# Kernel tuning notes

Measured on AMD Instinct MI355X. Metric: run time of the kernel, lower is better.

## Reference

```python
import jax, jax.numpy as jnp
import numpy as np

OUT_FEATURES = 4096
IN_FEATURES = 4096
GROUP_SIZE = 256
NUM_GROUPS = OUT_FEATURES * IN_FEATURES // GROUP_SIZE  # 65536


def setup_inputs() -> dict:
    key = jax.random.key(0)
    k1, k2, k3 = jax.random.split(key, 3)
    x = jax.random.normal(k1, (4, 2048, IN_FEATURES), dtype=jnp.float32)
    weight_packed = jax.random.randint(k2, (NUM_GROUPS, GROUP_SIZE // 2), 0, 256, dtype=jnp.int32)
    # params[..., 0] = scale, params[..., 1] = zero_point; keep scales small like real quant params
    weight_params = jax.random.uniform(k3, (NUM_GROUPS, 2), dtype=jnp.float32) * jnp.array([0.01, 0.1], dtype=jnp.float32)
    return {"x": x, "weight_packed": weight_packed, "weight_params": weight_params}


def _dequantize_4bit(weight_packed, weight_params):
    # weight_packed: [G, gs/2] bytes, two 4-bit values per byte (low nibble = even index)
    scales = weight_params[:, 0:1]  # [G, 1]
    zeros = weight_params[:, 1:2]   # [G, 1]
    low = (weight_packed & 15).astype(jnp.float32)          # even positions
    high = ((weight_packed >> 4) & 15).astype(jnp.float32)  # odd positions
    q = jnp.stack([low, high], axis=-1).reshape(weight_packed.shape[0], -1)  # [G, gs]
    return q * scales + zeros


def reference(x, weight_packed, weight_params):
    w = _dequantize_4bit(weight_packed, weight_params)  # [G, gs]
    w = w.reshape(-1)[: OUT_FEATURES * IN_FEATURES].reshape(OUT_FEATURES, IN_FEATURES)
    # F.linear(x, W) = x @ W.T
    return jnp.einsum("bsi,oi->bso", x, w)
```

## Files before the change

kernel.cpp:

```cpp
#include <hip/hip_runtime.h>
#include <hip/hip_bf16.h>


#define M_DIM 8192
#define N_DIM 4096
#define K_DIM 4096

typedef __bf16 bf16x8 __attribute__((ext_vector_type(8)));
typedef float f32x4 __attribute__((ext_vector_type(4)));
typedef unsigned short us8 __attribute__((ext_vector_type(8)));

__device__ __forceinline__ unsigned short f2bf_rne(float f) {
    unsigned int u = __builtin_bit_cast(unsigned int, f);
    u += 0x7FFFu + ((u >> 16) & 1u);
    return (unsigned short)(u >> 16);
}

__global__ void prep_kernel(const float* __restrict__ x,
                            const int* __restrict__ packed,
                            const float* __restrict__ params,
                            ushort* __restrict__ a,
                            ushort* __restrict__ w) {
    int b = blockIdx.x;
    if (b < 16384) {
        int j = b * 256 + threadIdx.x;
        float4 v0 = ((const float4*)x)[2 * j];
        float4 v1 = ((const float4*)x)[2 * j + 1];
        us8 o;
        o[0] = f2bf_rne(v0.x); o[1] = f2bf_rne(v0.y);
        o[2] = f2bf_rne(v0.z); o[3] = f2bf_rne(v0.w);
        o[4] = f2bf_rne(v1.x); o[5] = f2bf_rne(v1.y);
        o[6] = f2bf_rne(v1.z); o[7] = f2bf_rne(v1.w);
        ((us8*)a)[j] = o;
    } else {
        int j = (b - 16384) * 256 + threadIdx.x;
        int4 v = ((const int4*)packed)[j];
        int g = j >> 5;
        float s = params[2 * g], z = params[2 * g + 1];
        unsigned int o0, o1, o2, o3;
        o0 = (unsigned int)f2bf_rne((float)(v.x & 15) * s + z)
           | ((unsigned int)f2bf_rne((float)((v.x >> 4) & 15) * s + z) << 16);
        o1 = (unsigned int)f2bf_rne((float)(v.y & 15) * s + z)
           | ((unsigned int)f2bf_rne((float)((v.y >> 4) & 15) * s + z) << 16);
        o2 = (unsigned int)f2bf_rne((float)(v.z & 15) * s + z)
           | ((unsigned int)f2bf_rne((float)((v.z >> 4) & 15) * s + z) << 16);
        o3 = (unsigned int)f2bf_rne((float)(v.w & 15) * s + z)
           | ((unsigned int)f2bf_rne((float)((v.w >> 4) & 15) * s + z) << 16);
        ((uint4*)w)[j] = make_uint4(o0, o1, o2, o3);
    }
}

__global__ __launch_bounds__(512, 2) void gemm_bt(const ushort* __restrict__ A,
                                                  const ushort* __restrict__ B,
                                                  float* __restrict__ C) {
    __shared__ ushort lds[65536];

    const int tid  = threadIdx.x;
    const int w    = tid >> 6;
    const int lane = tid & 63;
    const int quad = lane >> 4;
    const int l16  = lane & 15;
    const int wm   = w >> 2;
    const int wn   = w & 3;

    const int bid = blockIdx.x;
    const int sid = (bid & 7) * 64 + (bid >> 3);
    const int by  = sid & 31;
    const int bx  = sid >> 5;
    const int m0  = by * 256;
    const int n0  = bx * 256;

    const int srow = tid >> 3;
    const int scol = ((tid & 7) ^ (srow & 7)) * 8;
    const ushort* aS = A + (size_t)(m0 + srow) * K_DIM + scol;
    const ushort* bS = B + (size_t)(n0 + srow) * K_DIM + scol;

    f32x4 acc[8][4] = {};
    bf16x8 afA[2][2], afB[2][2];
    bf16x8 bf0a[4], bf0b[4];
    bf16x8 bf1[4];

    auto stageA = [&](int t, int h) {
        const int kc   = (t < 64 ? t : 63) * 64;
        const int slot = ((t & 1) * 2 + h) * 8192;
#pragma unroll
        for (int l = 0; l < 2; ++l)
            __builtin_amdgcn_global_load_lds(
                (const __attribute__((address_space(1))) void*)(aS + (size_t)(h * 128 + l * 64) * K_DIM + kc),
                (__attribute__((address_space(3))) void*)(lds + slot + (l * 512 + w * 64) * 8),
                16, 0, 0);
    };
    auto stageB = [&](int t, int h) {
        const int kc   = (t < 64 ? t : 63) * 64;
        const int slot = 32768 + ((t & 1) * 2 + h) * 8192;
#pragma unroll
        for (int l = 0; l < 2; ++l)
            __builtin_amdgcn_global_load_lds(
                (const __attribute__((address_space(1))) void*)(bS + (size_t)(h * 128 + l * 64) * K_DIM + kc),
                (__attribute__((address_space(3))) void*)(lds + slot + (l * 512 + w * 64) * 8),
                16, 0, 0);
    };

    const int aBase = wm * 8192;
    const int bBase = 32768 + (wn >> 1) * 8192;
    const int bR0   = (wn & 1) * 64;
    const int swz8  = l16 & 7;
    const int c0    = (quad ^ swz8) * 8;
    const int c1    = ((4 + quad) ^ swz8) * 8;
    const ushort* pA0 = lds + aBase + l16 * 64 + c0;
    const ushort* pA1 = lds + aBase + l16 * 64 + c1;
    const ushort* pB0 = lds + bBase + (bR0 + l16) * 64 + c0;
    const ushort* pB1 = lds + bBase + (bR0 + l16) * 64 + c1;

#define MFMA_PH(PH, AF, BF0)                                                   \
    do {                                                                       \
        __builtin_amdgcn_s_setprio(1);                                         \
        _Pragma("unroll")                                                      \
        for (int ii = 0; ii < 2; ++ii)                                         \
            _Pragma("unroll")                                                  \
            for (int j = 0; j < 4; ++j)                                        \
                acc[(PH) * 2 + ii][j] = __builtin_amdgcn_mfma_f32_16x16x32_bf16( \
                    AF[ii][0], BF0[j], acc[(PH) * 2 + ii][j], 0, 0, 0);        \
        _Pragma("unroll")                                                      \
        for (int ii = 0; ii < 2; ++ii)                                         \
            _Pragma("unroll")                                                  \
            for (int j = 0; j < 4; ++j)                                        \
                acc[(PH) * 2 + ii][j] = __builtin_amdgcn_mfma_f32_16x16x32_bf16( \
                    AF[ii][1], bf1[j], acc[(PH) * 2 + ii][j], 0, 0, 0);        \
        __builtin_amdgcn_s_setprio(0);                                         \
    } while (0)

#define READ_A(DST, BUF, PH)                                                   \
    do {                                                                       \
        _Pragma("unroll")                                                      \
        for (int ii = 0; ii < 2; ++ii) {                                       \
            DST[ii][0] = *(const bf16x8*)(pA0 + (BUF) + ((PH) * 32 + ii * 16) * 64); \
            DST[ii][1] = *(const bf16x8*)(pA1 + (BUF) + ((PH) * 32 + ii * 16) * 64); \
        }                                                                      \
    } while (0)
#define READ_B0(DST, BUF)                                                      \
    do {                                                                       \
        _Pragma("unroll")                                                      \
        for (int j = 0; j < 4; ++j)                                            \
            DST[j] = *(const bf16x8*)(pB0 + (BUF) + j * 1024);                 \
    } while (0)
#define READ_B1(BUF)                                                           \
    do {                                                                       \
        _Pragma("unroll")                                                      \
        for (int j = 0; j < 4; ++j)                                            \
            bf1[j] = *(const bf16x8*)(pB1 + (BUF) + j * 1024);                 \
    } while (0)

    stageB(0, 0); stageB(0, 1); stageA(0, 0); stageA(0, 1); stageB(1, 0); stageB(1, 1);
    asm volatile("s_waitcnt vmcnt(4)" ::: "memory");
    __builtin_amdgcn_s_barrier();
    asm volatile("" ::: "memory");
    READ_B0(bf0a, 0);
    READ_A(afA, 0, 0);

#define TILE(T, BUF, NBUF, BF0C, BF0N)                                         \
    do {                                                                       \
        const int t = (T);                                                     \
                                                                      \
        READ_B1(BUF);                                                          \
        READ_A(afB, BUF, 1);                                                   \
        stageA(t + 1, 0);                                                      \
        MFMA_PH(0, afA, BF0C);                                                 \
                                                                      \
        READ_A(afA, BUF, 2);                                                   \
        stageA(t + 1, 1);                                                      \
        MFMA_PH(1, afB, BF0C);                                                 \
        asm volatile("s_waitcnt lgkmcnt(8)" ::: "memory");  \
        __builtin_amdgcn_sched_barrier(0);                  \
        __builtin_amdgcn_s_barrier();                 \
        asm volatile("" ::: "memory");                                         \
                                                                      \
        READ_A(afB, BUF, 3);                                                   \
        stageB(t + 2, 0);                                                      \
        MFMA_PH(2, afA, BF0C);                                                 \
                                                                      \
        stageB(t + 2, 1);                                                      \
        asm volatile("s_waitcnt vmcnt(4) lgkmcnt(0)" ::: "memory");            \
        __builtin_amdgcn_s_barrier();                \
        asm volatile("" ::: "memory");                                         \
        if (t < 63) { READ_B0(BF0N, NBUF); READ_A(afA, NBUF, 0); }             \
        __builtin_amdgcn_sched_barrier(0);                                     \
        MFMA_PH(3, afB, BF0C);                                                 \
    } while (0)

#pragma unroll 1
    for (int tt = 0; tt < 64; tt += 2) {
        TILE(tt,     0,     16384, bf0a, bf0b);
        TILE(tt + 1, 16384, 0,     bf0b, bf0a);
    }
#undef TILE
#undef MFMA_PH
#undef READ_A
#undef READ_B0
#undef READ_B1

    const int crow = m0 + wm * 128 + quad * 4;
    const int ccol = n0 + wn * 64 + l16;
#pragma unroll
    for (int rf = 0; rf < 8; ++rf)
#pragma unroll
        for (int j = 0; j < 4; ++j)
#pragma unroll
            for (int r = 0; r < 4; ++r)
                C[(size_t)(crow + rf * 16 + r) * N_DIM + ccol + j * 16] = acc[rf][j][r];
}

__global__ void naive_kernel(const float* __restrict__ x, const int* __restrict__ packed,
                             const float* __restrict__ params, float* __restrict__ out) {
    int idx = blockIdx.x * blockDim.x + threadIdx.x;
    if (idx >= M_DIM * N_DIM) return;
    int m = idx / N_DIM, o = idx % N_DIM;
    const float* xr = x + (size_t)m * K_DIM;
    float sum = 0.f;
    for (int gi = 0; gi < K_DIM / 256; ++gi) {
        int g = o * (K_DIM / 256) + gi;
        float s = params[2 * g], z = params[2 * g + 1];
        const int* p = packed + (size_t)g * 128;
        const float* xx = xr + gi * 256;
        for (int j = 0; j < 128; ++j) {
            int v = p[j];
            sum += xx[2 * j]     * ((float)(v & 15) * s + z);
            sum += xx[2 * j + 1] * ((float)((v >> 4) & 15) * s + z);
        }
    }
    out[idx] = sum;
}

extern "C" void kernel_launch(void* const* d_in, const int* in_sizes, int n_in,
                              void* d_out, int out_size, void* d_ws, size_t ws_size,
                              hipStream_t stream) {
    const float* x      = (const float*)d_in[0];
    const int*   packed = (const int*)d_in[1];
    const float* params = (const float*)d_in[2];
    float* out = (float*)d_out;

    const size_t a_bytes = (size_t)M_DIM * K_DIM * 2;
    const size_t w_bytes = (size_t)N_DIM * K_DIM * 2;

    if (ws_size >= a_bytes + w_bytes) {
        ushort* Abf = (ushort*)d_ws;
        ushort* Wbf = (ushort*)((char*)d_ws + a_bytes);

        prep_kernel<<<24576, 256, 0, stream>>>(x, packed, params, Abf, Wbf);

        gemm_bt<<<512, 512, 0, stream>>>(Abf, Wbf, out);
    } else {
        int n = M_DIM * N_DIM;
        naive_kernel<<<(n + 255) / 256, 256, 0, stream>>>(x, packed, params, out);
    }
}
```

Before: 455.9 us.

## Switch GEMM inner loop from 16x16x32 to 32x32x16 bf16 MFMA tiles

Replaces the 16x16x32 MFMA fragments with 32x32x16 bf16 MFMA, restructuring per-wave fragments into 4x2 accumulators of 16 floats and reorganizing LDS reads per K-substep. The larger MFMA shape reduces the number of LDS fragment loads and MFMA issues per unit of work, giving each fragment more reuse. It changes register usage and the waitcnt counts. The epilogue store layout also changes to match the 32x32 output layout.

```diff
diff --git a/kernel.cpp b/kernel.cpp
--- a/kernel.cpp
+++ b/kernel.cpp
@@ -7,7 +7,7 @@
 #define K_DIM 4096
 
 typedef __bf16 bf16x8 __attribute__((ext_vector_type(8)));
-typedef float f32x4 __attribute__((ext_vector_type(4)));
+typedef float f32x16 __attribute__((ext_vector_type(16)));
 typedef unsigned short us8 __attribute__((ext_vector_type(8)));
 
 __device__ __forceinline__ unsigned short f2bf_rne(float f) {
@@ -58,8 +58,8 @@
     const int tid  = threadIdx.x;
     const int w    = tid >> 6;
     const int lane = tid & 63;
-    const int quad = lane >> 4;
-    const int l16  = lane & 15;
+    const int r32  = lane & 31;
+    const int hi   = lane >> 5;
     const int wm   = w >> 2;
     const int wn   = w & 3;
 
@@ -75,10 +75,10 @@
     const ushort* aS = A + (size_t)(m0 + srow) * K_DIM + scol;
     const ushort* bS = B + (size_t)(n0 + srow) * K_DIM + scol;
 
-    f32x4 acc[8][4] = {};
-    bf16x8 afA[2][2], afB[2][2];
-    bf16x8 bf0a[4], bf0b[4];
-    bf16x8 bf1[4];
+    f32x16 acc[4][2] = {};
+    bf16x8 afA[4], afB[4];
+    bf16x8 bf0a[2], bf0b[2];
+    bf16x8 bfk[3][2];
 
     auto stageA = [&](int t, int h) {
         const int kc   = (t < 64 ? t : 63) * 64;
@@ -104,51 +104,48 @@
     const int aBase = wm * 8192;
     const int bBase = 32768 + (wn >> 1) * 8192;
     const int bR0   = (wn & 1) * 64;
-    const int swz8  = l16 & 7;
-    const int c0    = (quad ^ swz8) * 8;
-    const int c1    = ((4 + quad) ^ swz8) * 8;
-    const ushort* pA0 = lds + aBase + l16 * 64 + c0;
-    const ushort* pA1 = lds + aBase + l16 * 64 + c1;
-    const ushort* pB0 = lds + bBase + (bR0 + l16) * 64 + c0;
-    const ushort* pB1 = lds + bBase + (bR0 + l16) * 64 + c1;
-
-#define MFMA_PH(PH, AF, BF0)                                                   \
+    const int swz   = lane & 7;
+    const ushort* pA[4];
+    const ushort* pB[4];
+#pragma unroll
+    for (int ks = 0; ks < 4; ++ks) {
+        const int c = ((ks * 2 + hi) ^ swz) * 8;
+        pA[ks] = lds + aBase + r32 * 64 + c;
+        pB[ks] = lds + bBase + (bR0 + r32) * 64 + c;
+    }
+
+#define MFMA_KS(AF, B0, B1)                                                    \
     do {                                                                       \
         __builtin_amdgcn_s_setprio(1);                                         \
         _Pragma("unroll")                                                      \
-        for (int ii = 0; ii < 2; ++ii)                                         \
-            _Pragma("unroll")                                                  \
-            for (int j = 0; j < 4; ++j)                                        \
-                acc[(PH) * 2 + ii][j] = __builtin_amdgcn_mfma_f32_16x16x32_bf16( \
-                    AF[ii][0], BF0[j], acc[(PH) * 2 + ii][j], 0, 0, 0);        \
+        for (int mi = 0; mi < 4; ++mi) {                                       \
+            acc[mi][0] = __builtin_amdgcn_mfma_f32_32x32x16_bf16(              \
+                AF[mi], B0, acc[mi][0], 0, 0, 0);                              \
+            acc[mi][1] = __builtin_amdgcn_mfma_f32_32x32x16_bf16(              \
+                AF[mi], B1, acc[mi][1], 0, 0, 0);                              \
+        }                                                                      \
+        __builtin_amdgcn_s_setprio(0);                                         \
+    } while (0)
+
+#define READ_A(DST, BUF, KS)                                                   \
+    do {                                                                       \
         _Pragma("unroll")                                                      \
-        for (int ii = 0; ii < 2; ++ii)                                         \
-            _Pragma("unroll")                                                  \
-            for (int j = 0; j < 4; ++j)                                        \
-                acc[(PH) * 2 + ii][j] = __builtin_amdgcn_mfma_f32_16x16x32_bf16( \
-                    AF[ii][1], bf1[j], acc[(PH) * 2 + ii][j], 0, 0, 0);        \
-        __builtin_amdgcn_s_setprio(0);                                         \
-    } while (0)
-
-#define READ_A(DST, BUF, PH)                                                   \
-    do {                                                                       \
-        _Pragma("unroll")                                                      \
-        for (int ii = 0; ii < 2; ++ii) {                                       \
-            DST[ii][0] = *(const bf16x8*)(pA0 + (BUF) + ((PH) * 32 + ii * 16) * 64); \
-            DST[ii][1] = *(const bf16x8*)(pA1 + (BUF) + ((PH) * 32 + ii * 16) * 64); \
-        }                                                                      \
+        for (int mi = 0; mi < 4; ++mi)                                         \
+            DST[mi] = *(const bf16x8*)(pA[KS] + (BUF) + mi * 2048);            \
     } while (0)
 #define READ_B0(DST, BUF)                                                      \
     do {                                                                       \
-        _Pragma("unroll")                                                      \
-        for (int j = 0; j < 4; ++j)                                            \
-            DST[j] = *(const bf16x8*)(pB0 + (BUF) + j * 1024);                 \
-    } while (0)
-#define READ_B1(BUF)                                                           \
-    do {                                                                       \
-        _Pragma("unroll")                                                      \
-        for (int j = 0; j < 4; ++j)                                            \
-            bf1[j] = *(const bf16x8*)(pB1 + (BUF) + j * 1024);                 \
+        DST[0] = *(const bf16x8*)(pB[0] + (BUF));                              \
+        DST[1] = *(const bf16x8*)(pB[0] + (BUF) + 2048);                       \
+    } while (0)
+#define READ_B123(BUF)                                                         \
+    do {                                                                       \
+        bfk[0][0] = *(const bf16x8*)(pB[1] + (BUF));                           \
+        bfk[0][1] = *(const bf16x8*)(pB[1] + (BUF) + 2048);                    \
+        bfk[1][0] = *(const bf16x8*)(pB[2] + (BUF));                           \
+        bfk[1][1] = *(const bf16x8*)(pB[2] + (BUF) + 2048);                    \
+        bfk[2][0] = *(const bf16x8*)(pB[3] + (BUF));                           \
+        bfk[2][1] = *(const bf16x8*)(pB[3] + (BUF) + 2048);                    \
     } while (0)
 
     stageB(0, 0); stageB(0, 1); stageA(0, 0); stageA(0, 1); stageB(1, 0); stageB(1, 1);
@@ -162,22 +159,22 @@
     do {                                                                       \
         const int t = (T);                                                     \
                                                                       \
-        READ_B1(BUF);                                                          \
+        READ_B123(BUF);                                                        \
         READ_A(afB, BUF, 1);                                                   \
         stageA(t + 1, 0);                                                      \
-        MFMA_PH(0, afA, BF0C);                                                 \
+        MFMA_KS(afA, BF0C[0], BF0C[1]);                                        \
                                                                       \
         READ_A(afA, BUF, 2);                                                   \
         stageA(t + 1, 1);                                                      \
-        MFMA_PH(1, afB, BF0C);                                                 \
-        asm volatile("s_waitcnt lgkmcnt(8)" ::: "memory");  \
+        MFMA_KS(afB, bfk[0][0], bfk[0][1]);                                    \
+        asm volatile("s_waitcnt lgkmcnt(4)" ::: "memory");  \
         __builtin_amdgcn_sched_barrier(0);                  \
         __builtin_amdgcn_s_barrier();                 \
         asm volatile("" ::: "memory");                                         \
                                                                       \
         READ_A(afB, BUF, 3);                                                   \
         stageB(t + 2, 0);                                                      \
-        MFMA_PH(2, afA, BF0C);                                                 \
+        MFMA_KS(afA, bfk[1][0], bfk[1][1]);                                    \
                                                                       \
         stageB(t + 2, 1);                                                      \
         asm volatile("s_waitcnt vmcnt(4) lgkmcnt(0)" ::: "memory");            \
@@ -185,7 +182,7 @@
         asm volatile("" ::: "memory");                                         \
         if (t < 63) { READ_B0(BF0N, NBUF); READ_A(afA, NBUF, 0); }             \
         __builtin_amdgcn_sched_barrier(0);                                     \
-        MFMA_PH(3, afB, BF0C);                                                 \
+        MFMA_KS(afB, bfk[2][0], bfk[2][1]);                                    \
     } while (0)
 
 #pragma unroll 1
@@ -194,20 +191,22 @@
         TILE(tt + 1, 16384, 0,     bf0b, bf0a);
     }
 #undef TILE
-#undef MFMA_PH
+#undef MFMA_KS
 #undef READ_A
 #undef READ_B0
-#undef READ_B1
-
-    const int crow = m0 + wm * 128 + quad * 4;
-    const int ccol = n0 + wn * 64 + l16;
-#pragma unroll
-    for (int rf = 0; rf < 8; ++rf)
-#pragma unroll
-        for (int j = 0; j < 4; ++j)
-#pragma unroll
-            for (int r = 0; r < 4; ++r)
-                C[(size_t)(crow + rf * 16 + r) * N_DIM + ccol + j * 16] = acc[rf][j][r];
+#undef READ_B123
+
+    const int ccol = n0 + wn * 64 + r32;
+    const int crow = m0 + wm * 128 + 4 * hi;
+#pragma unroll
+    for (int mi = 0; mi < 4; ++mi)
+#pragma unroll
+        for (int nj = 0; nj < 2; ++nj)
+#pragma unroll
+            for (int reg = 0; reg < 16; ++reg) {
+                const int row = crow + mi * 32 + (reg & 3) + 8 * (reg >> 2);
+                C[(size_t)row * N_DIM + ccol + nj * 32] = acc[mi][nj][reg];
+            }
 }
 
 __global__ void naive_kernel(const float* __restrict__ x, const int* __restrict__ packed,
```

After: 472.3 us. 3.6% more time.
